# Performance work log

Hardware: AMD Instinct MI355X
Metric: run time of the kernel (lower is better)

Reference implementation:

```python
import jax, jax.numpy as jnp
import numpy as np

C_IN, C_KEY, C_VAL, C_OUT = 256, 128, 128, 256
B, H, W = 4, 64, 64
BN_EPS = 1e-5


def conv1x1(x, w, b):
    # x: [B,C,H,W], w: [O,C], b: [O]
    return jnp.einsum('bchw,oc->bohw', x, w) + b[None, :, None, None]


def bn_relu(x, gamma, beta, mean, var):
    inv = jax.lax.rsqrt(var + BN_EPS)
    y = (x - mean[None, :, None, None]) * (gamma * inv)[None, :, None, None] + beta[None, :, None, None]
    return jax.nn.relu(y)


def setup_inputs() -> dict:
    key = jax.random.key(0)
    ks = jax.random.split(key, 16)
    s = 0.05
    return {
        'x_enc': jax.random.normal(ks[0], (B, C_IN, H, W), jnp.float32),
        'x_dec': jax.random.normal(ks[1], (B, C_IN, H, W), jnp.float32),
        # f_key: conv + BN params
        'wk': jax.random.normal(ks[2], (C_KEY, C_IN), jnp.float32) * s,
        'bk': jax.random.normal(ks[3], (C_KEY,), jnp.float32) * s,
        'gk': jax.random.uniform(ks[4], (C_KEY,), jnp.float32, 0.5, 1.5),
        'betak': jax.random.normal(ks[5], (C_KEY,), jnp.float32) * s,
        'mk': jax.random.normal(ks[6], (C_KEY,), jnp.float32) * s,
        'vk': jax.random.uniform(ks[7], (C_KEY,), jnp.float32, 0.5, 1.5),
        # f_query: conv + BN params
        'wq': jax.random.normal(ks[8], (C_KEY, C_IN), jnp.float32) * s,
        'bq': jax.random.normal(ks[9], (C_KEY,), jnp.float32) * s,
        'gq': jax.random.uniform(ks[10], (C_KEY,), jnp.float32, 0.5, 1.5),
        'betaq': jax.random.normal(ks[11], (C_KEY,), jnp.float32) * s,
        'mq': jax.random.normal(ks[12], (C_KEY,), jnp.float32) * s,
        'vq': jax.random.uniform(ks[13], (C_KEY,), jnp.float32, 0.5, 1.5),
        # f_value conv
        'wv': jax.random.normal(ks[14], (C_VAL, C_IN), jnp.float32) * s,
        'bv': jnp.zeros((C_VAL,), jnp.float32),
        # output projection W (random instead of zero-init to avoid degenerate baseline)
        'wo': jax.random.normal(ks[15], (C_OUT, C_VAL), jnp.float32) * s,
        'bo': jnp.zeros((C_OUT,), jnp.float32),
    }


def reference(x_enc, x_dec, wk, bk, gk, betak, mk, vk, wq, bq, gq, betaq, mq, vq, wv, bv, wo, bo):
    b, _, h, w = x_enc.shape
    hw = h * w
    # value: [B, HW, Cv]
    value = conv1x1(x_enc, wv, bv).reshape(b, C_VAL, hw).transpose(0, 2, 1)
    # query: [B, HW, Ck]
    query = bn_relu(conv1x1(x_dec, wq, bq), gq, betaq, mq, vq).reshape(b, C_KEY, hw).transpose(0, 2, 1)
    # key: [B, Ck, HW]
    key = bn_relu(conv1x1(x_enc, wk, bk), gk, betak, mk, vk).reshape(b, C_KEY, hw)
    sim = jnp.einsum('bqc,bck->bqk', query, key) * (C_KEY ** -0.5)  # [B, HW, HW]
    attn = jax.nn.softmax(sim, axis=-1)
    context = jnp.einsum('bqk,bkc->bqc', attn, value)  # [B, HW, Cv]
    context = context.transpose(0, 2, 1).reshape(b, C_VAL, h, w)
    return conv1x1(context, wo, bo)
```

## Files before the change

kernel.cpp:

```cpp
#include <hip/hip_runtime.h>

typedef __attribute__((ext_vector_type(8))) short short8;
typedef __attribute__((ext_vector_type(4))) float floatx4;

#define HW 4096
#define CIN 256
#define CK 128
#define COUT 256
#define NB 4
#define BN_EPS 1e-5f
#define SC2 0.12751744526f

#define MFMA(a, b, c) __builtin_amdgcn_mfma_f32_16x16x32_bf16((a), (b), (c), 0, 0, 0)

__device__ __forceinline__ unsigned short f2bf(float f) {
  union { float f; unsigned u; } v; v.f = f;
  unsigned r = v.u + 0x7fffu + ((v.u >> 16) & 1u);
  return (unsigned short)(r >> 16);
}

__device__ __forceinline__ unsigned bfr(float f) {
  union { float f; unsigned u; } v; v.f = f;
  return v.u + 0x7fffu + ((v.u >> 16) & 1u);
}

__device__ __forceinline__ unsigned pack2(float a, float b) {
  return (bfr(a) >> 16) | (bfr(b) & 0xffff0000u);
}

__device__ __forceinline__ float bf2f(unsigned short u) {
  union { unsigned u; float f; } v; v.u = ((unsigned)u) << 16;
  return v.f;
}

__device__ __forceinline__ short8 pack8(const float* p) {
  short8 r;
#pragma unroll
  for (int i = 0; i < 8; ++i) r[i] = (short)f2bf(p[i]);
  return r;
}

__global__ __launch_bounds__(256) void prep_kernel(
    const float* __restrict__ wq, const float* __restrict__ wk,
    const float* __restrict__ wv, const float* __restrict__ wo,
    unsigned short* __restrict__ WqP, unsigned short* __restrict__ WkvP,
    unsigned short* __restrict__ WoP)
{
  const int t = blockIdx.x * 256 + threadIdx.x;
  float tmp[8];
  if (t < 4096) {
    const int lane = t & 63, mt = (t >> 6) & 1, wave = (t >> 7) & 3, ks = t >> 9;
    const int lane16 = lane & 15, quad = lane >> 4;
    const int o = wave * 32 + mt * 16 + lane16;
    const float* src = wq + (size_t)o * CIN + ks * 32 + quad * 8;
    *(float4*)tmp = *(const float4*)src;
    *(float4*)(tmp + 4) = *(const float4*)(src + 4);
    *(short8*)&WqP[(size_t)t * 8] = pack8(tmp);
  } else if (t < 12288) {
    const int u = t - 4096;
    const int lane = u & 63, mt = (u >> 6) & 3, wave = (u >> 8) & 3, ks = u >> 10;
    const int lane16 = lane & 15, quad = lane >> 4;
    const int o = wave * 64 + mt * 16 + lane16;
    const float* row = (o < 128) ? wk + (size_t)o * CIN : wv + (size_t)(o - 128) * CIN;
    const float* src = row + ks * 32 + quad * 8;
    *(float4*)tmp = *(const float4*)src;
    *(float4*)(tmp + 4) = *(const float4*)(src + 4);
    *(short8*)&WkvP[(size_t)u * 8] = pack8(tmp);
  } else {
    const int u = t - 12288;
    const int lane = u & 63, mt = (u >> 6) & 3, wave = (u >> 8) & 3, ks = u >> 10;
    const int lane16 = lane & 15, quad = lane >> 4;
    const int o = wave * 64 + mt * 16 + lane16;
    const float* src = wo + (size_t)o * CK + ks * 32 + quad * 8;
    *(float4*)tmp = *(const float4*)src;
    *(float4*)(tmp + 4) = *(const float4*)(src + 4);
    *(short8*)&WoP[(size_t)u * 8] = pack8(tmp);
  }
}

__global__ __launch_bounds__(256) void proj_kernel(
    const float* __restrict__ x_enc, const float* __restrict__ x_dec,
    const unsigned short* __restrict__ WqP, const unsigned short* __restrict__ WkvP,
    const float* __restrict__ bq, const float* __restrict__ gq,
    const float* __restrict__ betaq, const float* __restrict__ mq,
    const float* __restrict__ vq,
    const float* __restrict__ bk, const float* __restrict__ gk,
    const float* __restrict__ betak, const float* __restrict__ mk,
    const float* __restrict__ vk, const float* __restrict__ bv,
    unsigned short* __restrict__ Qb, unsigned short* __restrict__ Kb,
    unsigned short* __restrict__ Vt)
{
  const int tid = threadIdx.x;
  const int pt = blockIdx.x;
  const int b  = blockIdx.y;
  const int pj = blockIdx.z;

  const float* X = (pj == 0) ? x_dec : x_enc;

  __shared__ float xF[64 * 68];
  __shared__ unsigned short xT[64 * 264];

  const float* Xs = X + (size_t)b * CIN * HW + (size_t)pt * 64;
#pragma unroll
  for (int qtr = 0; qtr < 4; ++qtr) {
    if (qtr) __syncthreads();
    {
      const int c = tid >> 2;
      const int p0 = (tid & 3) * 16;
      const float* src = Xs + (size_t)(qtr * 64 + c) * HW + p0;
#pragma unroll
      for (int j = 0; j < 4; ++j)
        *(float4*)&xF[c * 68 + p0 + j * 4] = *(const float4*)(src + j * 4);
    }
    __syncthreads();
    {
      const int p = tid & 63;
      const int cb = tid >> 6;
#pragma unroll
      for (int jj = 0; jj < 2; ++jj) {
        const int c0 = (jj * 4 + cb) * 8;
        float t[8];
#pragma unroll
        for (int u = 0; u < 8; ++u) t[u] = xF[(c0 + u) * 68 + p];
        *(short8*)&xT[p * 264 + qtr * 64 + c0] = pack8(t);
      }
    }
  }
  __syncthreads();

  const int wave = tid >> 6;
  const int lane = tid & 63;
  const int lane16 = lane & 15;
  const int quad = lane >> 4;

  if (pj == 0) {
    floatx4 acc[2][4];
#pragma unroll
    for (int mt = 0; mt < 2; ++mt)
#pragma unroll
      for (int nf = 0; nf < 4; ++nf) acc[mt][nf] = (floatx4){0.f, 0.f, 0.f, 0.f};

#pragma unroll
    for (int ks = 0; ks < 8; ++ks) {
      short8 af[2];
#pragma unroll
      for (int mt = 0; mt < 2; ++mt)
        af[mt] = *(const short8*)&WqP[(size_t)((((ks * 4 + wave) * 2 + mt) * 64) + lane) * 8];
#pragma unroll
      for (int nf = 0; nf < 4; ++nf) {
        const short8 bf = *(const short8*)&xT[(nf * 16 + lane16) * 264 + ks * 32 + quad * 8];
#pragma unroll
        for (int mt = 0; mt < 2; ++mt) acc[mt][nf] = MFMA(af[mt], bf, acc[mt][nf]);
      }
    }

    float sc[2][4], off[2][4];
#pragma unroll
    for (int mt = 0; mt < 2; ++mt)
#pragma unroll
      for (int r = 0; r < 4; ++r) {
        const int o = wave * 32 + mt * 16 + quad * 4 + r;
        const float s = gq[o] * rsqrtf(vq[o] + BN_EPS) * SC2;
        sc[mt][r] = s;
        off[mt][r] = (bq[o] - mq[o]) * s + betaq[o] * SC2;
      }
#pragma unroll
    for (int nf = 0; nf < 4; ++nf) {
      const size_t prow = ((size_t)b * HW + pt * 64 + nf * 16 + lane16) * CK;
#pragma unroll
      for (int mt = 0; mt < 2; ++mt) {
        ushort4 pk;
        pk.x = f2bf(fmaxf(acc[mt][nf][0] * sc[mt][0] + off[mt][0], 0.f));
        pk.y = f2bf(fmaxf(acc[mt][nf][1] * sc[mt][1] + off[mt][1], 0.f));
        pk.z = f2bf(fmaxf(acc[mt][nf][2] * sc[mt][2] + off[mt][2], 0.f));
        pk.w = f2bf(fmaxf(acc[mt][nf][3] * sc[mt][3] + off[mt][3], 0.f));
        *(ushort4*)(Qb + prow + wave * 32 + mt * 16 + quad * 4) = pk;
      }
    }
  } else {
    const bool isK = (wave < 2);
    floatx4 acc[4][4];
#pragma unroll
    for (int mt = 0; mt < 4; ++mt)
#pragma unroll
      for (int nf = 0; nf < 4; ++nf) acc[mt][nf] = (floatx4){0.f, 0.f, 0.f, 0.f};

#pragma unroll
    for (int ks = 0; ks < 8; ++ks) {
      short8 af[4];
#pragma unroll
      for (int mt = 0; mt < 4; ++mt)
        af[mt] = *(const short8*)&WkvP[(size_t)((((ks * 4 + wave) * 4 + mt) * 64) + lane) * 8];
#pragma unroll
      for (int nf = 0; nf < 4; ++nf) {
        const short8 bf = *(const short8*)&xT[(nf * 16 + lane16) * 264 + ks * 32 + quad * 8];
#pragma unroll
        for (int mt = 0; mt < 4; ++mt) acc[mt][nf] = MFMA(af[mt], bf, acc[mt][nf]);
      }
    }

    if (isK) {
      float sc[4][4], off[4][4];
#pragma unroll
      for (int mt = 0; mt < 4; ++mt)
#pragma unroll
        for (int r = 0; r < 4; ++r) {
          const int o = wave * 64 + mt * 16 + quad * 4 + r;
          const float s = gk[o] * rsqrtf(vk[o] + BN_EPS);
          sc[mt][r] = s;
          off[mt][r] = (bk[o] - mk[o]) * s + betak[o];
        }
#pragma unroll
      for (int nf = 0; nf < 4; ++nf) {
        const size_t prow = ((size_t)b * HW + pt * 64 + nf * 16 + lane16) * CK;
#pragma unroll
        for (int mt = 0; mt < 4; ++mt) {
          ushort4 pk;
          pk.x = f2bf(fmaxf(acc[mt][nf][0] * sc[mt][0] + off[mt][0], 0.f));
          pk.y = f2bf(fmaxf(acc[mt][nf][1] * sc[mt][1] + off[mt][1], 0.f));
          pk.z = f2bf(fmaxf(acc[mt][nf][2] * sc[mt][2] + off[mt][2], 0.f));
          pk.w = f2bf(fmaxf(acc[mt][nf][3] * sc[mt][3] + off[mt][3], 0.f));
          *(ushort4*)(Kb + prow + wave * 64 + mt * 16 + quad * 4) = pk;
        }
      }
    } else {
#pragma unroll
      for (int mt = 0; mt < 4; ++mt) {
#pragma unroll
        for (int r = 0; r < 4; ++r) {
          const int c = wave * 64 + mt * 16 + quad * 4 + r - 128;
          const float bias = bv[c];
          unsigned short* dst = Vt + ((size_t)(b * CK + c)) * HW + pt * 64;
#pragma unroll
          for (int nf = 0; nf < 4; ++nf)
            dst[nf * 16 + lane16] = f2bf(acc[mt][nf][r] + bias);
        }
      }
    }
  }
}

template<int NKC>
__global__ __launch_bounds__(256, 2) void attn_kernel8(
    const unsigned short* __restrict__ Qb, const unsigned short* __restrict__ Kb,
    const unsigned short* __restrict__ Vt, unsigned short* __restrict__ OpartH,
    float* __restrict__ Ml)
{
  constexpr int ITERS = 64 / NKC;
  const int tid = threadIdx.x;
  const int blk = blockIdx.x;
  const int b  = blk & 3;
  const int qt = (blk >> 2) & 31;
  const int kc = blk >> 7;

  const int wave = tid >> 6;
  const int lane = tid & 63;
  const int lane16 = lane & 15;
  const int quad = lane >> 4;

  __shared__ unsigned short Kl[64 * 136];
  __shared__ unsigned short Vl[128 * 72];
  __shared__ unsigned short Pl[4][32 * 72];
  unsigned short* Pw = &Pl[wave][0];

  const int q0 = qt * 128 + wave * 32;
  short8 qf[2][4];
  {
    const unsigned short* Qs = Qb + ((size_t)b * HW + q0) * CK;
#pragma unroll
    for (int mt = 0; mt < 2; ++mt)
#pragma unroll
      for (int ks = 0; ks < 4; ++ks)
        qf[mt][ks] = *(const short8*)(Qs + (size_t)(mt * 16 + lane16) * CK + ks * 32 + quad * 8);
  }

  short8 ones;
#pragma unroll
  for (int i = 0; i < 8; ++i) ones[i] = (short)0x3F80;

  floatx4 O[2][8];
  floatx4 Lacc[2];
#pragma unroll
  for (int mt = 0; mt < 2; ++mt) {
    Lacc[mt] = (floatx4){0.f, 0.f, 0.f, 0.f};
#pragma unroll
    for (int nf = 0; nf < 8; ++nf) O[mt][nf] = (floatx4){0.f, 0.f, 0.f, 0.f};
  }

  const int krow = tid >> 4;
  const int kcol = (tid & 15) * 8;
  const int vrow = tid >> 1;
  const int vcol = (tid & 1) * 32;

  const unsigned short* Kg = Kb + (size_t)b * HW * CK + (size_t)(kc * ITERS * 64) * CK;
  const unsigned short* Vg = Vt + (size_t)b * CK * HW + kc * ITERS * 64;

  short8 kr[4], vr[4];
#pragma unroll
  for (int i2 = 0; i2 < 4; ++i2)
    kr[i2] = *(const short8*)(Kg + (size_t)(krow + i2 * 16) * CK + kcol);
#pragma unroll
  for (int i2 = 0; i2 < 4; ++i2)
    vr[i2] = *(const short8*)(Vg + (size_t)vrow * HW + vcol + i2 * 8);

  for (int it = 0; it < ITERS; ++it) {
    __syncthreads();
#pragma unroll
    for (int i2 = 0; i2 < 4; ++i2)
      *(short8*)&Kl[(krow + i2 * 16) * 136 + kcol] = kr[i2];
#pragma unroll
    for (int i2 = 0; i2 < 4; ++i2)
      *(short8*)&Vl[vrow * 72 + vcol + i2 * 8] = vr[i2];
    __syncthreads();

    if (it + 1 < ITERS) {
      const unsigned short* Kn = Kg + (size_t)((it + 1) * 64) * CK;
      const unsigned short* Vn = Vg + (it + 1) * 64;
#pragma unroll
      for (int i2 = 0; i2 < 4; ++i2)
        kr[i2] = *(const short8*)(Kn + (size_t)(krow + i2 * 16) * CK + kcol);
#pragma unroll
      for (int i2 = 0; i2 < 4; ++i2)
        vr[i2] = *(const short8*)(Vn + (size_t)vrow * HW + vcol + i2 * 8);
    }

#pragma unroll
    for (int nf = 0; nf < 4; ++nf) {
      floatx4 s0 = (floatx4){0.f, 0.f, 0.f, 0.f};
      floatx4 s1 = (floatx4){0.f, 0.f, 0.f, 0.f};
#pragma unroll
      for (int ks = 0; ks < 4; ++ks) {
        const short8 kf = *(const short8*)&Kl[(nf * 16 + lane16) * 136 + ks * 32 + quad * 8];
        s0 = MFMA(kf, qf[0][ks], s0);
        s1 = MFMA(kf, qf[1][ks], s1);
      }
      const int kcol8 = nf * 16 + quad * 4;
      *(uint2*)&Pw[lane16 * 72 + kcol8] = make_uint2(
          pack2(__builtin_amdgcn_exp2f(s0[0]), __builtin_amdgcn_exp2f(s0[1])),
          pack2(__builtin_amdgcn_exp2f(s0[2]), __builtin_amdgcn_exp2f(s0[3])));
      *(uint2*)&Pw[(16 + lane16) * 72 + kcol8] = make_uint2(
          pack2(__builtin_amdgcn_exp2f(s1[0]), __builtin_amdgcn_exp2f(s1[1])),
          pack2(__builtin_amdgcn_exp2f(s1[2]), __builtin_amdgcn_exp2f(s1[3])));
    }
    __threadfence_block();

#pragma unroll
    for (int ks = 0; ks < 2; ++ks) {
      const int colr = ks * 32 + quad * 8;
      const short8 pf0 = *(const short8*)&Pw[lane16 * 72 + colr];
      const short8 pf1 = *(const short8*)&Pw[(16 + lane16) * 72 + colr];
      Lacc[0] = MFMA(pf0, ones, Lacc[0]);
      Lacc[1] = MFMA(pf1, ones, Lacc[1]);
#pragma unroll
      for (int nf = 0; nf < 8; ++nf) {
        const short8 vf = *(const short8*)&Vl[(nf * 16 + lane16) * 72 + ks * 32 + quad * 8];
        O[0][nf] = MFMA(pf0, vf, O[0][nf]);
        O[1][nf] = MFMA(pf1, vf, O[1][nf]);
      }
    }
  }

  const int chunk = (b * 32 + qt) * NKC + kc;
  unsigned short* Op = OpartH + (size_t)chunk * (128 * 128);
#pragma unroll
  for (int mt = 0; mt < 2; ++mt)
#pragma unroll
    for (int nf = 0; nf < 8; ++nf)
#pragma unroll
      for (int r = 0; r < 4; ++r)
        Op[(size_t)(wave * 32 + mt * 16 + quad * 4 + r) * 128 + nf * 16 + lane16] =
            f2bf(O[mt][nf][r]);
  if (lane16 == 0) {
    float* Mp = Ml + (size_t)chunk * 128 + wave * 32;
#pragma unroll
    for (int mt = 0; mt < 2; ++mt)
#pragma unroll
      for (int r = 0; r < 4; ++r)
        Mp[mt * 16 + quad * 4 + r] = Lacc[mt][r];
  }
}

template<int NKC>
__global__ __launch_bounds__(256) void outproj_kernel(
    const unsigned short* __restrict__ OpartH, const float* __restrict__ Ml,
    const unsigned short* __restrict__ WoP, const float* __restrict__ bo,
    float* __restrict__ out)
{
  const int tid = threadIdx.x;
  const int pt = blockIdx.x;
  const int b  = blockIdx.y;
  const int qt = pt >> 3;
  const int q0 = (pt & 7) * 16;
  const int chunk0 = (b * 32 + qt) * NKC;

  __shared__ unsigned short Ctile[16 * 136];

  {
    const int row = tid >> 4;
    const int c8  = (tid & 15) * 8;
    float L = 0.f;
#pragma unroll
    for (int k = 0; k < NKC; ++k) L += Ml[(size_t)(chunk0 + k) * 128 + q0 + row];
    float acc[8];
#pragma unroll
    for (int i = 0; i < 8; ++i) acc[i] = 0.f;
#pragma unroll
    for (int k = 0; k < NKC; ++k) {
      const short8 v = *(const short8*)(OpartH + (size_t)(chunk0 + k) * 16384 +
                                        (size_t)(q0 + row) * 128 + c8);
#pragma unroll
      for (int i = 0; i < 8; ++i) acc[i] += bf2f((unsigned short)v[i]);
    }
    const float inv = 1.f / L;
#pragma unroll
    for (int i = 0; i < 8; ++i) acc[i] *= inv;
    *(short8*)&Ctile[row * 136 + c8] = pack8(acc);
  }
  __syncthreads();

  const int wave = tid >> 6;
  const int lane = tid & 63;
  const int lane16 = lane & 15;
  const int quad = lane >> 4;

  floatx4 acc[4];
#pragma unroll
  for (int mt = 0; mt < 4; ++mt) acc[mt] = (floatx4){0.f, 0.f, 0.f, 0.f};

#pragma unroll
  for (int ks = 0; ks < 4; ++ks) {
    const short8 bf = *(const short8*)&Ctile[lane16 * 136 + ks * 32 + quad * 8];
#pragma unroll
    for (int mt = 0; mt < 4; ++mt) {
      const short8 af = *(const short8*)&WoP[(size_t)((((ks * 4 + wave) * 4 + mt) * 64) + lane) * 8];
      acc[mt] = MFMA(af, bf, acc[mt]);
    }
  }

#pragma unroll
  for (int mt = 0; mt < 4; ++mt) {
#pragma unroll
    for (int r = 0; r < 4; ++r) {
      const int o = wave * 64 + mt * 16 + quad * 4 + r;
      float* dst = out + ((size_t)b * COUT + o) * HW + qt * 128 + q0;
      dst[lane16] = acc[mt][r] + bo[o];
    }
  }
}

extern "C" void kernel_launch(void* const* d_in, const int* in_sizes, int n_in,
                              void* d_out, int out_size, void* d_ws, size_t ws_size,
                              hipStream_t stream)
{
  (void)in_sizes; (void)n_in; (void)out_size;
  const float* x_enc = (const float*)d_in[0];
  const float* x_dec = (const float*)d_in[1];
  const float* wk    = (const float*)d_in[2];
  const float* bk    = (const float*)d_in[3];
  const float* gk    = (const float*)d_in[4];
  const float* betak = (const float*)d_in[5];
  const float* mk    = (const float*)d_in[6];
  const float* vk    = (const float*)d_in[7];
  const float* wq    = (const float*)d_in[8];
  const float* bq    = (const float*)d_in[9];
  const float* gq    = (const float*)d_in[10];
  const float* betaq = (const float*)d_in[11];
  const float* mq    = (const float*)d_in[12];
  const float* vq    = (const float*)d_in[13];
  const float* wv    = (const float*)d_in[14];
  const float* bv    = (const float*)d_in[15];
  const float* wo    = (const float*)d_in[16];
  const float* bo    = (const float*)d_in[17];
  float* out = (float*)d_out;

  const size_t qkv = (size_t)NB * HW * CK;
  unsigned short* WqP  = (unsigned short*)d_ws;
  unsigned short* WkvP = WqP + 32768;
  unsigned short* WoP  = WkvP + 65536;
  unsigned short* Qb   = WoP + 32768;
  unsigned short* Kb   = Qb + qkv;
  unsigned short* Vt   = Kb + qkv;
  unsigned short* OpartH = Vt + qkv;
  const size_t fixed_bytes = 131072 * 2 + 3 * qkv * 2;

  prep_kernel<<<dim3(64), 256, 0, stream>>>(wq, wk, wv, wo, WqP, WkvP, WoP);
  proj_kernel<<<dim3(64, 4, 2), 256, 0, stream>>>(
      x_enc, x_dec, WqP, WkvP,
      bq, gq, betaq, mq, vq, bk, gk, betak, mk, vk, bv, Qb, Kb, Vt);

  auto need = [&](int nkc) {
    return fixed_bytes + (size_t)128 * nkc * 16384 * 2
                       + (size_t)128 * nkc * 128 * 4;
  };
  if (ws_size >= need(8)) {
    float* Ml = (float*)(OpartH + (size_t)128 * 8 * 16384);
    attn_kernel8<8><<<dim3(1024), 256, 0, stream>>>(Qb, Kb, Vt, OpartH, Ml);
    outproj_kernel<8><<<dim3(256, 4), 256, 0, stream>>>(OpartH, Ml, WoP, bo, out);
  } else if (ws_size >= need(4)) {
    float* Ml = (float*)(OpartH + (size_t)128 * 4 * 16384);
    attn_kernel8<4><<<dim3(512), 256, 0, stream>>>(Qb, Kb, Vt, OpartH, Ml);
    outproj_kernel<4><<<dim3(256, 4), 256, 0, stream>>>(OpartH, Ml, WoP, bo, out);
  } else if (ws_size >= need(2)) {
    float* Ml = (float*)(OpartH + (size_t)128 * 2 * 16384);
    attn_kernel8<2><<<dim3(256), 256, 0, stream>>>(Qb, Kb, Vt, OpartH, Ml);
    outproj_kernel<2><<<dim3(256, 4), 256, 0, stream>>>(OpartH, Ml, WoP, bo, out);
  } else {
    float* Ml = (float*)(OpartH + (size_t)128 * 1 * 16384);
    attn_kernel8<1><<<dim3(128), 256, 0, stream>>>(Qb, Kb, Vt, OpartH, Ml);
    outproj_kernel<1><<<dim3(256, 4), 256, 0, stream>>>(OpartH, Ml, WoP, bo, out);
  }
}
```

Baseline: 170.3 us.

## Keep softmax probabilities in registers using 16x16x16 MFMA, drop LDS P staging

The QK^T accumulator layout is fed straight as the A operand of 16x16x16 bf16 MFMAs for the PV product and row sums. This removes the per-wave LDS buffer for P along with its write/fence/read round trip. It also raises the launch-bounds occupancy hint from 2 to 4 blocks per SM, which may constrain registers and cause spills. The K=16 MFMA issues twice as many instructions as the K=32 form for the same work.

```diff
diff --git a/kernel.cpp b/kernel.cpp
--- a/kernel.cpp
+++ b/kernel.cpp
@@ -1,6 +1,7 @@
 #include <hip/hip_runtime.h>
 
 typedef __attribute__((ext_vector_type(8))) short short8;
+typedef __attribute__((ext_vector_type(4))) short short4v;
 typedef __attribute__((ext_vector_type(4))) float floatx4;
 
 #define HW 4096
@@ -12,6 +13,7 @@
 #define SC2 0.12751744526f
 
 #define MFMA(a, b, c) __builtin_amdgcn_mfma_f32_16x16x32_bf16((a), (b), (c), 0, 0, 0)
+#define MFMA16(a, b, c) __builtin_amdgcn_mfma_f32_16x16x16bf16_1k((a), (b), (c), 0, 0, 0)
 
 __device__ __forceinline__ unsigned short f2bf(float f) {
   union { float f; unsigned u; } v; v.f = f;
@@ -241,7 +243,7 @@
 }
 
 template<int NKC>
-__global__ __launch_bounds__(256, 2) void attn_kernel8(
+__global__ __launch_bounds__(256, 4) void attn_kernel8(
     const unsigned short* __restrict__ Qb, const unsigned short* __restrict__ Kb,
     const unsigned short* __restrict__ Vt, unsigned short* __restrict__ OpartH,
     float* __restrict__ Ml)
@@ -260,8 +262,6 @@
 
   __shared__ unsigned short Kl[64 * 136];
   __shared__ unsigned short Vl[128 * 72];
-  __shared__ unsigned short Pl[4][32 * 72];
-  unsigned short* Pw = &Pl[wave][0];
 
   const int q0 = qt * 128 + wave * 32;
   short8 qf[2][4];
@@ -274,9 +274,9 @@
         qf[mt][ks] = *(const short8*)(Qs + (size_t)(mt * 16 + lane16) * CK + ks * 32 + quad * 8);
   }
 
-  short8 ones;
-#pragma unroll
-  for (int i = 0; i < 8; ++i) ones[i] = (short)0x3F80;
+  short4v ones4;
+#pragma unroll
+  for (int i = 0; i < 4; ++i) ones4[i] = (short)0x3F80;
 
   floatx4 O[2][8];
   floatx4 Lacc[2];
@@ -334,28 +334,21 @@
         s0 = MFMA(kf, qf[0][ks], s0);
         s1 = MFMA(kf, qf[1][ks], s1);
       }
-      const int kcol8 = nf * 16 + quad * 4;
-      *(uint2*)&Pw[lane16 * 72 + kcol8] = make_uint2(
-          pack2(__builtin_amdgcn_exp2f(s0[0]), __builtin_amdgcn_exp2f(s0[1])),
-          pack2(__builtin_amdgcn_exp2f(s0[2]), __builtin_amdgcn_exp2f(s0[3])));
-      *(uint2*)&Pw[(16 + lane16) * 72 + kcol8] = make_uint2(
-          pack2(__builtin_amdgcn_exp2f(s1[0]), __builtin_amdgcn_exp2f(s1[1])),
-          pack2(__builtin_amdgcn_exp2f(s1[2]), __builtin_amdgcn_exp2f(s1[3])));
-    }
-    __threadfence_block();
-
-#pragma unroll
-    for (int ks = 0; ks < 2; ++ks) {
-      const int colr = ks * 32 + quad * 8;
-      const short8 pf0 = *(const short8*)&Pw[lane16 * 72 + colr];
-      const short8 pf1 = *(const short8*)&Pw[(16 + lane16) * 72 + colr];
-      Lacc[0] = MFMA(pf0, ones, Lacc[0]);
-      Lacc[1] = MFMA(pf1, ones, Lacc[1]);
-#pragma unroll
-      for (int nf = 0; nf < 8; ++nf) {
-        const short8 vf = *(const short8*)&Vl[(nf * 16 + lane16) * 72 + ks * 32 + quad * 8];
-        O[0][nf] = MFMA(pf0, vf, O[0][nf]);
-        O[1][nf] = MFMA(pf1, vf, O[1][nf]);
+      union { unsigned u[2]; short4v s; } pa0, pa1;
+      pa0.u[0] = pack2(__builtin_amdgcn_exp2f(s0[0]), __builtin_amdgcn_exp2f(s0[1]));
+      pa0.u[1] = pack2(__builtin_amdgcn_exp2f(s0[2]), __builtin_amdgcn_exp2f(s0[3]));
+      pa1.u[0] = pack2(__builtin_amdgcn_exp2f(s1[0]), __builtin_amdgcn_exp2f(s1[1]));
+      pa1.u[1] = pack2(__builtin_amdgcn_exp2f(s1[2]), __builtin_amdgcn_exp2f(s1[3]));
+
+      Lacc[0] = MFMA16(pa0.s, ones4, Lacc[0]);
+      Lacc[1] = MFMA16(pa1.s, ones4, Lacc[1]);
+
+      const int vcol8 = nf * 16 + quad * 4;
+#pragma unroll
+      for (int cb = 0; cb < 8; ++cb) {
+        const short4v vf = *(const short4v*)&Vl[(cb * 16 + lane16) * 72 + vcol8];
+        O[0][cb] = MFMA16(pa0.s, vf, O[0][cb]);
+        O[1][cb] = MFMA16(pa1.s, vf, O[1][cb]);
       }
     }
   }
```

Result: slower. 299.7 us (+76.0%).

## Alias K and P shared buffers and drop register prefetch for higher occupancy

Applied to the files above, without the earlier changes.

The attention kernel now reuses one LDS buffer for both the K tile and the per-wave P tiles, with an extra barrier between the score computation and the P writes. It also removes the register-held prefetch of the next K/V tile, loading directly before the store to LDS, and raises the launch bound from 2 to 4 blocks per SM. The aim is to cut LDS and register use so more blocks fit on each CU and hide latency that way. The cost is that global-load latency is no longer overlapped inside a block, and each iteration adds a barrier.

```diff
diff --git a/kernel.cpp b/kernel.cpp
--- a/kernel.cpp
+++ b/kernel.cpp
@@ -241,7 +241,7 @@
 }
 
 template<int NKC>
-__global__ __launch_bounds__(256, 2) void attn_kernel8(
+__global__ __launch_bounds__(256, 4) void attn_kernel8(
     const unsigned short* __restrict__ Qb, const unsigned short* __restrict__ Kb,
     const unsigned short* __restrict__ Vt, unsigned short* __restrict__ OpartH,
     float* __restrict__ Ml)
@@ -258,10 +258,10 @@
   const int lane16 = lane & 15;
   const int quad = lane >> 4;
 
-  __shared__ unsigned short Kl[64 * 136];
+  __shared__ unsigned short KP[4 * 32 * 72];
   __shared__ unsigned short Vl[128 * 72];
-  __shared__ unsigned short Pl[4][32 * 72];
-  unsigned short* Pw = &Pl[wave][0];
+  unsigned short* Kl = KP;
+  unsigned short* Pw = KP + wave * (32 * 72);
 
   const int q0 = qt * 128 + wave * 32;
   short8 qf[2][4];
@@ -292,38 +292,31 @@
   const int vrow = tid >> 1;
   const int vcol = (tid & 1) * 32;
 
-  const unsigned short* Kg = Kb + (size_t)b * HW * CK + (size_t)(kc * ITERS * 64) * CK;
+  const unsigned short* Kg = Kb + ((size_t)b * HW + (size_t)kc * ITERS * 64) * CK;
   const unsigned short* Vg = Vt + (size_t)b * CK * HW + kc * ITERS * 64;
-
-  short8 kr[4], vr[4];
-#pragma unroll
-  for (int i2 = 0; i2 < 4; ++i2)
-    kr[i2] = *(const short8*)(Kg + (size_t)(krow + i2 * 16) * CK + kcol);
-#pragma unroll
-  for (int i2 = 0; i2 < 4; ++i2)
-    vr[i2] = *(const short8*)(Vg + (size_t)vrow * HW + vcol + i2 * 8);
 
   for (int it = 0; it < ITERS; ++it) {
     __syncthreads();
-#pragma unroll
-    for (int i2 = 0; i2 < 4; ++i2)
-      *(short8*)&Kl[(krow + i2 * 16) * 136 + kcol] = kr[i2];
-#pragma unroll
-    for (int i2 = 0; i2 < 4; ++i2)
-      *(short8*)&Vl[vrow * 72 + vcol + i2 * 8] = vr[i2];
-    __syncthreads();
-
-    if (it + 1 < ITERS) {
-      const unsigned short* Kn = Kg + (size_t)((it + 1) * 64) * CK;
-      const unsigned short* Vn = Vg + (it + 1) * 64;
+    {
+      const unsigned short* Kn = Kg + (size_t)(it * 64) * CK;
+      const unsigned short* Vn = Vg + it * 64;
+      short8 kr[4], vr[4];
 #pragma unroll
       for (int i2 = 0; i2 < 4; ++i2)
         kr[i2] = *(const short8*)(Kn + (size_t)(krow + i2 * 16) * CK + kcol);
 #pragma unroll
       for (int i2 = 0; i2 < 4; ++i2)
         vr[i2] = *(const short8*)(Vn + (size_t)vrow * HW + vcol + i2 * 8);
-    }
-
+#pragma unroll
+      for (int i2 = 0; i2 < 4; ++i2)
+        *(short8*)&Kl[(krow + i2 * 16) * 136 + kcol] = kr[i2];
+#pragma unroll
+      for (int i2 = 0; i2 < 4; ++i2)
+        *(short8*)&Vl[vrow * 72 + vcol + i2 * 8] = vr[i2];
+    }
+    __syncthreads();
+
+    unsigned preg[4][4];
 #pragma unroll
     for (int nf = 0; nf < 4; ++nf) {
       floatx4 s0 = (floatx4){0.f, 0.f, 0.f, 0.f};
@@ -334,13 +327,18 @@
         s0 = MFMA(kf, qf[0][ks], s0);
         s1 = MFMA(kf, qf[1][ks], s1);
       }
+      preg[nf][0] = pack2(__builtin_amdgcn_exp2f(s0[0]), __builtin_amdgcn_exp2f(s0[1]));
+      preg[nf][1] = pack2(__builtin_amdgcn_exp2f(s0[2]), __builtin_amdgcn_exp2f(s0[3]));
+      preg[nf][2] = pack2(__builtin_amdgcn_exp2f(s1[0]), __builtin_amdgcn_exp2f(s1[1]));
+      preg[nf][3] = pack2(__builtin_amdgcn_exp2f(s1[2]), __builtin_amdgcn_exp2f(s1[3]));
+    }
+    __syncthreads();
+
+#pragma unroll
+    for (int nf = 0; nf < 4; ++nf) {
       const int kcol8 = nf * 16 + quad * 4;
-      *(uint2*)&Pw[lane16 * 72 + kcol8] = make_uint2(
-          pack2(__builtin_amdgcn_exp2f(s0[0]), __builtin_amdgcn_exp2f(s0[1])),
-          pack2(__builtin_amdgcn_exp2f(s0[2]), __builtin_amdgcn_exp2f(s0[3])));
-      *(uint2*)&Pw[(16 + lane16) * 72 + kcol8] = make_uint2(
-          pack2(__builtin_amdgcn_exp2f(s1[0]), __builtin_amdgcn_exp2f(s1[1])),
-          pack2(__builtin_amdgcn_exp2f(s1[2]), __builtin_amdgcn_exp2f(s1[3])));
+      *(uint2*)&Pw[lane16 * 72 + kcol8]        = make_uint2(preg[nf][0], preg[nf][1]);
+      *(uint2*)&Pw[(16 + lane16) * 72 + kcol8] = make_uint2(preg[nf][2], preg[nf][3]);
     }
     __threadfence_block();
 
```

Result: slower. 247.4 us (+45.3%).

## Keep softmax probabilities in registers by permuting K rows in LDS

Applied to the files above, without the earlier changes.

Removes the per-wave LDS staging buffer for the exponentiated scores. K rows are written to shared memory in a permuted order so that the QK^T MFMA output layout of each lane lines up with the A-operand layout the PV MFMA needs. The bf16 probabilities can then be packed straight from the accumulators into the operand registers. This drops LDS writes and reads plus a block fence per iteration, in exchange for more live accumulators (four score tiles at once) and a subtle permutation that has to stay consistent with V's column order.

```diff
diff --git a/kernel.cpp b/kernel.cpp
--- a/kernel.cpp
+++ b/kernel.cpp
@@ -260,8 +260,6 @@
 
   __shared__ unsigned short Kl[64 * 136];
   __shared__ unsigned short Vl[128 * 72];
-  __shared__ unsigned short Pl[4][32 * 72];
-  unsigned short* Pw = &Pl[wave][0];
 
   const int q0 = qt * 128 + wave * 32;
   short8 qf[2][4];
@@ -292,7 +290,14 @@
   const int vrow = tid >> 1;
   const int vcol = (tid & 1) * 32;
 
-  const unsigned short* Kg = Kb + (size_t)b * HW * CK + (size_t)(kc * ITERS * 64) * CK;
+  int kslot[4];
+#pragma unroll
+  for (int i2 = 0; i2 < 4; ++i2) {
+    const int g = krow + i2 * 16;
+    kslot[i2] = (g & 0x23) | ((g & 0x18) >> 1) | ((g & 0x04) << 2);
+  }
+
+  const unsigned short* Kg = Kb + ((size_t)b * HW + (size_t)kc * ITERS * 64) * CK;
   const unsigned short* Vg = Vt + (size_t)b * CK * HW + kc * ITERS * 64;
 
   short8 kr[4], vr[4];
@@ -307,7 +312,7 @@
     __syncthreads();
 #pragma unroll
     for (int i2 = 0; i2 < 4; ++i2)
-      *(short8*)&Kl[(krow + i2 * 16) * 136 + kcol] = kr[i2];
+      *(short8*)&Kl[kslot[i2] * 136 + kcol] = kr[i2];
 #pragma unroll
     for (int i2 = 0; i2 < 4; ++i2)
       *(short8*)&Vl[vrow * 72 + vcol + i2 * 8] = vr[i2];
@@ -325,37 +330,37 @@
     }
 
 #pragma unroll
-    for (int nf = 0; nf < 4; ++nf) {
-      floatx4 s0 = (floatx4){0.f, 0.f, 0.f, 0.f};
-      floatx4 s1 = (floatx4){0.f, 0.f, 0.f, 0.f};
+    for (int kp = 0; kp < 2; ++kp) {
+      floatx4 sA0 = (floatx4){0.f, 0.f, 0.f, 0.f};
+      floatx4 sA1 = (floatx4){0.f, 0.f, 0.f, 0.f};
+      floatx4 sB0 = (floatx4){0.f, 0.f, 0.f, 0.f};
+      floatx4 sB1 = (floatx4){0.f, 0.f, 0.f, 0.f};
 #pragma unroll
       for (int ks = 0; ks < 4; ++ks) {
-        const short8 kf = *(const short8*)&Kl[(nf * 16 + lane16) * 136 + ks * 32 + quad * 8];
-        s0 = MFMA(kf, qf[0][ks], s0);
-        s1 = MFMA(kf, qf[1][ks], s1);
-      }
-      const int kcol8 = nf * 16 + quad * 4;
-      *(uint2*)&Pw[lane16 * 72 + kcol8] = make_uint2(
-          pack2(__builtin_amdgcn_exp2f(s0[0]), __builtin_amdgcn_exp2f(s0[1])),
-          pack2(__builtin_amdgcn_exp2f(s0[2]), __builtin_amdgcn_exp2f(s0[3])));
-      *(uint2*)&Pw[(16 + lane16) * 72 + kcol8] = make_uint2(
-          pack2(__builtin_amdgcn_exp2f(s1[0]), __builtin_amdgcn_exp2f(s1[1])),
-          pack2(__builtin_amdgcn_exp2f(s1[2]), __builtin_amdgcn_exp2f(s1[3])));
-    }
-    __threadfence_block();
-
-#pragma unroll
-    for (int ks = 0; ks < 2; ++ks) {
-      const int colr = ks * 32 + quad * 8;
-      const short8 pf0 = *(const short8*)&Pw[lane16 * 72 + colr];
-      const short8 pf1 = *(const short8*)&Pw[(16 + lane16) * 72 + colr];
-      Lacc[0] = MFMA(pf0, ones, Lacc[0]);
-      Lacc[1] = MFMA(pf1, ones, Lacc[1]);
+        const short8 kfA = *(const short8*)&Kl[((2 * kp) * 16 + lane16) * 136 + ks * 32 + quad * 8];
+        const short8 kfB = *(const short8*)&Kl[((2 * kp + 1) * 16 + lane16) * 136 + ks * 32 + quad * 8];
+        sA0 = MFMA(kfA, qf[0][ks], sA0);
+        sA1 = MFMA(kfA, qf[1][ks], sA1);
+        sB0 = MFMA(kfB, qf[0][ks], sB0);
+        sB1 = MFMA(kfB, qf[1][ks], sB1);
+      }
+      union { unsigned u[4]; short8 s; } pf0, pf1;
+      pf0.u[0] = pack2(__builtin_amdgcn_exp2f(sA0[0]), __builtin_amdgcn_exp2f(sA0[1]));
+      pf0.u[1] = pack2(__builtin_amdgcn_exp2f(sA0[2]), __builtin_amdgcn_exp2f(sA0[3]));
+      pf0.u[2] = pack2(__builtin_amdgcn_exp2f(sB0[0]), __builtin_amdgcn_exp2f(sB0[1]));
+      pf0.u[3] = pack2(__builtin_amdgcn_exp2f(sB0[2]), __builtin_amdgcn_exp2f(sB0[3]));
+      pf1.u[0] = pack2(__builtin_amdgcn_exp2f(sA1[0]), __builtin_amdgcn_exp2f(sA1[1]));
+      pf1.u[1] = pack2(__builtin_amdgcn_exp2f(sA1[2]), __builtin_amdgcn_exp2f(sA1[3]));
+      pf1.u[2] = pack2(__builtin_amdgcn_exp2f(sB1[0]), __builtin_amdgcn_exp2f(sB1[1]));
+      pf1.u[3] = pack2(__builtin_amdgcn_exp2f(sB1[2]), __builtin_amdgcn_exp2f(sB1[3]));
+
+      Lacc[0] = MFMA(pf0.s, ones, Lacc[0]);
+      Lacc[1] = MFMA(pf1.s, ones, Lacc[1]);
 #pragma unroll
       for (int nf = 0; nf < 8; ++nf) {
-        const short8 vf = *(const short8*)&Vl[(nf * 16 + lane16) * 72 + ks * 32 + quad * 8];
-        O[0][nf] = MFMA(pf0, vf, O[0][nf]);
-        O[1][nf] = MFMA(pf1, vf, O[1][nf]);
+        const short8 vf = *(const short8*)&Vl[(nf * 16 + lane16) * 72 + kp * 32 + quad * 8];
+        O[0][nf] = MFMA(pf0.s, vf, O[0][nf]);
+        O[1][nf] = MFMA(pf1.s, vf, O[1][nf]);
       }
     }
   }
```

Result: no change. 167.9 us (-1.4%).
